# Kernel tuning notes

Measured on AMD Instinct MI355X. Metric: run time of the kernel, lower is better.

Reference implementation:

```python
import jax, jax.numpy as jnp
import numpy as np

HIDDEN = 1024
HEADS = 16
HEAD_DIM = HIDDEN // HEADS  # 64
B, S = 4, 2048


def setup_inputs() -> dict:
    key = jax.random.key(0)
    ks = jax.random.split(key, 8)
    scale = 1.0 / np.sqrt(HIDDEN)
    return {
        "hidden_states": jax.random.normal(ks[0], (B, S, HIDDEN), dtype=jnp.float32),
        "attention_mask": jnp.zeros((B, S), dtype=jnp.float32),  # additive mask: 0 = keep
        "Wq": jax.random.normal(ks[1], (HIDDEN, HIDDEN), dtype=jnp.float32) * scale,
        "bq": jnp.zeros((HIDDEN,), dtype=jnp.float32),
        "Wk": jax.random.normal(ks[2], (HIDDEN, HIDDEN), dtype=jnp.float32) * scale,
        "bk": jnp.zeros((HIDDEN,), dtype=jnp.float32),
        "Wv": jax.random.normal(ks[3], (HIDDEN, HIDDEN), dtype=jnp.float32) * scale,
        "bv": jnp.zeros((HIDDEN,), dtype=jnp.float32),
    }


def reference(hidden_states, attention_mask, Wq, bq, Wk, bk, Wv, bv):
    b, s, _ = hidden_states.shape

    def split_heads(x):  # [b,s,hidden] -> [b,h,s,d]
        return x.reshape(b, s, HEADS, HEAD_DIM).transpose(0, 2, 1, 3)

    q = split_heads(hidden_states @ Wq + bq)
    k = split_heads(hidden_states @ Wk + bk)
    v = split_heads(hidden_states @ Wv + bv)

    # [b,h,s,s] attention scores, scaled, with additive mask broadcast to [b,1,1,s]
    scores = jnp.einsum("bhqd,bhkd->bhqk", q, k) / np.sqrt(HEAD_DIM)
    scores = scores + attention_mask[:, None, None, :]
    probs = jax.nn.softmax(scores, axis=-1)
    # dropout prob = 0 (eval); head_mask=None
    ctx = jnp.einsum("bhqk,bhkd->bhqd", probs, v)  # [b,h,s,d]
    return ctx.transpose(0, 2, 1, 3).reshape(b, s, HIDDEN)
```

## Files before the change

kernel.cpp:

```cpp
#include <hip/hip_runtime.h>
#include <hip/hip_bf16.h>

typedef unsigned short u16t;
typedef unsigned int   u32t;
typedef float  f32x4  __attribute__((ext_vector_type(4)));
typedef __bf16 bf16x8 __attribute__((ext_vector_type(8)));

#define HIDDEN 1024
#define HEADS  16
#define HDIM   64
#define BB     4
#define SS     2048
#define BH     (BB * HEADS)
#define MTOT   (BB * SS)
#define LOG2E  1.4426950408889634f

__device__ inline u16t f2bf(float f) {
  __hip_bfloat16 h = __float2bfloat16(f);
  return *reinterpret_cast<u16t*>(&h);
}

__device__ inline float fast_exp2(float x) {
#if __has_builtin(__builtin_amdgcn_exp2f)
  return __builtin_amdgcn_exp2f(x);
#else
  return exp2f(x);
#endif
}

__device__ inline void gload_lds16(const void* g, void* l) {
  __builtin_amdgcn_global_load_lds(
      (const __attribute__((address_space(1))) void*)g,
      (__attribute__((address_space(3))) void*)l, 16, 0, 0);
}

__global__ __launch_bounds__(256) void k_convert_x(const float* __restrict__ X,
                                                   u16t* __restrict__ Xb, int n4) {
  int i = blockIdx.x * blockDim.x + threadIdx.x;
  int stride = gridDim.x * blockDim.x;
  for (; i < n4; i += stride) {
    float4 v = reinterpret_cast<const float4*>(X)[i];
    ushort4 o;
    o.x = f2bf(v.x); o.y = f2bf(v.y); o.z = f2bf(v.z); o.w = f2bf(v.w);
    reinterpret_cast<ushort4*>(Xb)[i] = o;
  }
}

__global__ __launch_bounds__(256) void k_transpose_w(const float* __restrict__ Wq,
                                                     const float* __restrict__ Wk,
                                                     const float* __restrict__ Wv,
                                                     u16t* __restrict__ Wt) {
  __shared__ float tile[64][65];
  const int mat = blockIdx.z;
  const float* W = (mat == 0) ? Wq : (mat == 1) ? Wk : Wv;
  const int k0 = blockIdx.x * 64, n0 = blockIdx.y * 64;
  const int t = threadIdx.x;
  const int c = t & 63, rbase = t >> 6;
#pragma unroll
  for (int p = 0; p < 16; ++p) {
    int r = p * 4 + rbase;
    tile[r][c] = W[(size_t)(k0 + r) * HIDDEN + n0 + c];
  }
  __syncthreads();
  u16t* Wo = Wt + (size_t)mat * HIDDEN * HIDDEN;
#pragma unroll
  for (int p = 0; p < 16; ++p) {
    int r = p * 4 + rbase;
    Wo[(size_t)(n0 + r) * HIDDEN + k0 + c] = f2bf(tile[c][r]);
  }
}

template <bool SWAP>
__global__ __launch_bounds__(256) void k_qkv_gemm(const u16t* __restrict__ Xb,
                                                  const u16t* __restrict__ Wt,
                                                  const float* __restrict__ bq,
                                                  const float* __restrict__ bk,
                                                  const float* __restrict__ bv,
                                                  u16t* __restrict__ QKV,
                                                  int n0base) {
  __shared__ __align__(16) u16t As[128 * 64];
  __shared__ __align__(16) u16t Bs[128 * 64];
  const int nwg = (int)(gridDim.x * gridDim.y);
  const int bid = (int)(blockIdx.x + gridDim.x * blockIdx.y);
  const int lg  = (bid & 7) * (nwg >> 3) + (bid >> 3);
  const int m0 = (lg & 63) * 128, n0 = n0base + (lg >> 6) * 128;
  const int tid = threadIdx.x;
  const int w = tid >> 6, l = tid & 63;
  const int lq = l & 15, g = l >> 4;
  const int wm = (w >> 1) * 64, wn = (w & 1) * 64;

  f32x4 acc[4][4] = {};

  for (int t = 0; t < 16; ++t) {
    const int k0 = t * 64;
    __syncthreads();
#pragma unroll
    for (int p = 0; p < 4; ++p) {
      int chunk = p * 256 + tid;
      int row = chunk >> 3, c16 = chunk & 7;
      int sc = ((c16 ^ (row & 7)) * 8);
      gload_lds16(Xb + (size_t)(m0 + row) * HIDDEN + k0 + sc,
                  &As[(p * 256 + w * 64) * 8]);
      gload_lds16(Wt + (size_t)(n0 + row) * HIDDEN + k0 + sc,
                  &Bs[(p * 256 + w * 64) * 8]);
    }
    __syncthreads();
#pragma unroll
    for (int kc = 0; kc < 2; ++kc) {
      bf16x8 af[4], bfr[4];
#pragma unroll
      for (int i = 0; i < 4; ++i) {
        int rowA = wm + i * 16 + lq;
        af[i] = *reinterpret_cast<const bf16x8*>(
            &As[rowA * 64 + (((kc * 4 + g) ^ (rowA & 7)) * 8)]);
        int rowB = wn + i * 16 + lq;
        bfr[i] = *reinterpret_cast<const bf16x8*>(
            &Bs[rowB * 64 + (((kc * 4 + g) ^ (rowB & 7)) * 8)]);
      }
#pragma unroll
      for (int i = 0; i < 4; ++i)
#pragma unroll
        for (int j = 0; j < 4; ++j) {
          if constexpr (SWAP)
            acc[i][j] = __builtin_amdgcn_mfma_f32_16x16x32_bf16(bfr[j], af[i],
                                                                acc[i][j], 0, 0, 0);
          else
            acc[i][j] = __builtin_amdgcn_mfma_f32_16x16x32_bf16(af[i], bfr[j],
                                                                acc[i][j], 0, 0, 0);
        }
    }
  }

  if constexpr (SWAP) {
    const int nb_ = n0 >> 10;
    const float* bias = nb_ ? bk : bq;
    const float scl = nb_ ? 1.0f : 0.125f * LOG2E;
#pragma unroll
    for (int j = 0; j < 4; ++j) {
      int nf = (n0 & 1023) + wn + j * 16 + g * 4;
      int h = nf >> 6, d0 = nf & 63;
      float4 b4 = *reinterpret_cast<const float4*>(&bias[nf]);
#pragma unroll
      for (int i = 0; i < 4; ++i) {
        int m = m0 + wm + i * 16 + lq;
        int b = m >> 11, s = m & 2047;
        ushort4 o;
        o.x = f2bf((acc[i][j][0] + b4.x) * scl);
        o.y = f2bf((acc[i][j][1] + b4.y) * scl);
        o.z = f2bf((acc[i][j][2] + b4.z) * scl);
        o.w = f2bf((acc[i][j][3] + b4.w) * scl);
        *reinterpret_cast<ushort4*>(
            &QKV[(((size_t)(nb_ * BH + b * HEADS + h)) * SS + s) * HDIM + d0]) = o;
      }
    }
  } else {
    u16t* Vg = QKV + (size_t)2 * BH * SS * HDIM;
#pragma unroll
    for (int j = 0; j < 4; ++j) {
      int n = (n0 - 2048) + wn + j * 16 + lq;
      int h = n >> 6, d = n & 63;
      float bval = bv[n];
#pragma unroll
      for (int i = 0; i < 4; ++i) {
        int m = m0 + wm + i * 16 + g * 4;
        int b = m >> 11, s = m & 2047;
        int tt = s >> 6, k = s & 63;
        int slot = (k & 32) + ((k >> 2) & 3) * 8 + ((k >> 4) & 1) * 4;
        ushort4 o;
        o.x = f2bf(acc[i][j][0] + bval);
        o.y = f2bf(acc[i][j][1] + bval);
        o.z = f2bf(acc[i][j][2] + bval);
        o.w = f2bf(acc[i][j][3] + bval);
        *reinterpret_cast<ushort4*>(
            &Vg[(((size_t)(b * HEADS + h)) * HDIM + d) * SS + tt * 64 + slot]) = o;
      }
    }
  }
}

__global__ __launch_bounds__(256) void k_attn(const u16t* __restrict__ QKV,
                                              const float* __restrict__ mask,
                                              float* __restrict__ out) {
  __shared__ __align__(16) u16t Ks[2][64 * 64];
  __shared__ __align__(16) u16t Vs[2][64 * 64];
  __shared__ float Ms[SS];
  const int bid = (int)(blockIdx.x + gridDim.x * blockIdx.y);
  const int lg  = (bid & 7) * 128 + (bid >> 3);
  const int qt = lg & 15, bh = lg >> 4;
  const int b = bh >> 4, h = bh & 15;
  const int tid = threadIdx.x, w = tid >> 6, l = tid & 63;
  const int lq = l & 15, g = l >> 4;
  const int q0 = qt * 128 + w * 32;

  const u16t* Qh = QKV + (size_t)bh * SS * HDIM;
  const u16t* Kh = QKV + (size_t)(BH + bh) * SS * HDIM;
  const u16t* Vh = QKV + (size_t)(2 * BH) * SS * HDIM + (size_t)bh * HDIM * SS;

  {
    const float4* m4 = reinterpret_cast<const float4*>(mask + (size_t)b * SS);
    float4* s4 = reinterpret_cast<float4*>(Ms);
    for (int i = tid; i < SS / 4; i += 256) {
      float4 v = m4[i];
      v.x = v.x * LOG2E - 8.0f; v.y = v.y * LOG2E - 8.0f;
      v.z = v.z * LOG2E - 8.0f; v.w = v.w * LOG2E - 8.0f;
      s4[i] = v;
    }
  }

  bf16x8 qf[2][2];
#pragma unroll
  for (int qi = 0; qi < 2; ++qi) {
    qf[qi][0] = *reinterpret_cast<const bf16x8*>(
        &Qh[(size_t)(q0 + qi * 16 + lq) * HDIM + g * 8]);
    qf[qi][1] = *reinterpret_cast<const bf16x8*>(
        &Qh[(size_t)(q0 + qi * 16 + lq) * HDIM + 32 + g * 8]);
  }

  const int cA = tid, cB = 256 + tid;
  const u16t* ksrcA = Kh + (size_t)(cA >> 3) * HDIM + (((cA & 7) ^ ((cA >> 3) & 7)) * 8);
  const u16t* ksrcB = Kh + (size_t)(cB >> 3) * HDIM + (((cB & 7) ^ ((cB >> 3) & 7)) * 8);
  const u16t* vsrcA = Vh + (size_t)(cA >> 3) * SS + (((cA & 7) ^ ((cA >> 3) & 7)) * 8);
  const u16t* vsrcB = Vh + (size_t)(cB >> 3) * SS + (((cB & 7) ^ ((cB >> 3) & 7)) * 8);

  auto STAGE = [&](int t, int bufi) {
    const size_t ko = (size_t)t * 64 * HDIM;
    const int vo = t * 64;
    gload_lds16(ksrcA + ko, &Ks[bufi][(w * 64) * 8]);
    gload_lds16(ksrcB + ko, &Ks[bufi][(256 + w * 64) * 8]);
    gload_lds16(vsrcA + vo, &Vs[bufi][(w * 64) * 8]);
    gload_lds16(vsrcB + vo, &Vs[bufi][(256 + w * 64) * 8]);
  };

  float lsum[2] = {0.f, 0.f};
  f32x4 ctx[2][4] = {};
  u32t pk[2][4][2];

  STAGE(0, 0);
  __syncthreads();

  for (int kv = 0; kv < 32; ++kv) {
    const int cur = kv & 1;
    const int k0 = kv * 64;
    STAGE((kv + 1) & 31, cur ^ 1);
    asm volatile("s_waitcnt vmcnt(4)\n\ts_barrier" ::: "memory");

    const u16t* Kb = &Ks[cur][0];
    const u16t* Vb = &Vs[cur][0];

    bf16x8 kf[4][2];
#pragma unroll
    for (int mt = 0; mt < 4; ++mt) {
      int row = mt * 16 + lq;
      kf[mt][0] = *reinterpret_cast<const bf16x8*>(
          &Kb[row * 64 + ((g ^ (row & 7)) * 8)]);
      kf[mt][1] = *reinterpret_cast<const bf16x8*>(
          &Kb[row * 64 + (((4 + g) ^ (row & 7)) * 8)]);
    }

    float4 mvs[4];
#pragma unroll
    for (int mt = 0; mt < 4; ++mt)
      mvs[mt] = *reinterpret_cast<const float4*>(&Ms[k0 + mt * 16 + g * 4]);

#pragma unroll
    for (int qi = 0; qi < 2; ++qi) {
      f32x4 s[4];
      __builtin_amdgcn_s_setprio(1);
#pragma unroll
      for (int mt = 0; mt < 4; ++mt) {
        f32x4 z = {};
        z = __builtin_amdgcn_mfma_f32_16x16x32_bf16(kf[mt][0], qf[qi][0], z, 0, 0, 0);
        z = __builtin_amdgcn_mfma_f32_16x16x32_bf16(kf[mt][1], qf[qi][1], z, 0, 0, 0);
        s[mt][0] = z[0] + mvs[mt].x; s[mt][1] = z[1] + mvs[mt].y;
        s[mt][2] = z[2] + mvs[mt].z; s[mt][3] = z[3] + mvs[mt].w;
      }
      __builtin_amdgcn_s_setprio(0);
      float ps = 0.f;
#pragma unroll
      for (int mt = 0; mt < 4; ++mt) {
        float p0 = fast_exp2(s[mt][0]), p1 = fast_exp2(s[mt][1]);
        float p2 = fast_exp2(s[mt][2]), p3 = fast_exp2(s[mt][3]);
        ps += (p0 + p1) + (p2 + p3);
        pk[qi][mt][0] = ((u32t)f2bf(p1) << 16) | f2bf(p0);
        pk[qi][mt][1] = ((u32t)f2bf(p3) << 16) | f2bf(p2);
      }
      lsum[qi] += ps;
    }

#pragma unroll
    for (int c = 0; c < 2; ++c) {
      union { u32t u[4]; bf16x8 v; } pb[2];
#pragma unroll
      for (int qi = 0; qi < 2; ++qi) {
        pb[qi].u[0] = pk[qi][2 * c][0];
        pb[qi].u[1] = pk[qi][2 * c][1];
        pb[qi].u[2] = pk[qi][2 * c + 1][0];
        pb[qi].u[3] = pk[qi][2 * c + 1][1];
      }
      __builtin_amdgcn_s_setprio(1);
#pragma unroll
      for (int dt = 0; dt < 4; ++dt) {
        int d = dt * 16 + lq;
        bf16x8 vf = *reinterpret_cast<const bf16x8*>(
            &Vb[d * 64 + (((4 * c + g) ^ (d & 7)) * 8)]);
        ctx[0][dt] = __builtin_amdgcn_mfma_f32_16x16x32_bf16(vf, pb[0].v, ctx[0][dt], 0, 0, 0);
        ctx[1][dt] = __builtin_amdgcn_mfma_f32_16x16x32_bf16(vf, pb[1].v, ctx[1][dt], 0, 0, 0);
      }
      __builtin_amdgcn_s_setprio(0);
    }

    asm volatile("s_barrier" ::: "memory");
  }

#pragma unroll
  for (int qi = 0; qi < 2; ++qi) {
    float ls = lsum[qi];
    ls += __shfl_xor(ls, 16);
    ls += __shfl_xor(ls, 32);
    float rinv = 1.0f / ls;
    int qg = q0 + qi * 16 + lq;
#pragma unroll
    for (int dt = 0; dt < 4; ++dt) {
      float4 o;
      o.x = ctx[qi][dt][0] * rinv; o.y = ctx[qi][dt][1] * rinv;
      o.z = ctx[qi][dt][2] * rinv; o.w = ctx[qi][dt][3] * rinv;
      *reinterpret_cast<float4*>(
          &out[((size_t)(b * SS + qg)) * HIDDEN + h * HDIM + dt * 16 + g * 4]) = o;
    }
  }
}

extern "C" void kernel_launch(void* const* d_in, const int* in_sizes, int n_in,
                              void* d_out, int out_size, void* d_ws, size_t ws_size,
                              hipStream_t stream) {
  const float* X    = (const float*)d_in[0];
  const float* mask = (const float*)d_in[1];
  const float* Wq   = (const float*)d_in[2];
  const float* bq   = (const float*)d_in[3];
  const float* Wk   = (const float*)d_in[4];
  const float* bk   = (const float*)d_in[5];
  const float* Wv   = (const float*)d_in[6];
  const float* bv   = (const float*)d_in[7];
  float* out = (float*)d_out;

  u16t* Xb  = (u16t*)d_ws;
  u16t* Wt  = Xb + (size_t)MTOT * HIDDEN;
  u16t* QKV = Wt + (size_t)3 * HIDDEN * HIDDEN;

  hipLaunchKernelGGL(k_convert_x, dim3(2048), dim3(256), 0, stream,
                     X, Xb, MTOT * HIDDEN / 4);
  hipLaunchKernelGGL(k_transpose_w, dim3(16, 16, 3), dim3(256), 0, stream,
                     Wq, Wk, Wv, Wt);
  hipLaunchKernelGGL((k_qkv_gemm<true>), dim3(64, 16), dim3(256), 0, stream,
                     Xb, Wt, bq, bk, bv, QKV, 0);
  hipLaunchKernelGGL((k_qkv_gemm<false>), dim3(64, 8), dim3(256), 0, stream,
                     Xb, Wt, bq, bk, bv, QKV, 2048);
  hipLaunchKernelGGL(k_attn, dim3(16, 64), dim3(256), 0, stream,
                     QKV, mask, out);
}
```

Measured before the change: 282.0 us.

## Merge QKV GEMM launches and compute softmax row sums with MFMA

New measurement: 274.9 us. 2.5% less time.

```diff
diff --git a/kernel.cpp b/kernel.cpp
--- a/kernel.cpp
+++ b/kernel.cpp
@@ -70,20 +70,19 @@
   }
 }
 
-template <bool SWAP>
 __global__ __launch_bounds__(256) void k_qkv_gemm(const u16t* __restrict__ Xb,
                                                   const u16t* __restrict__ Wt,
                                                   const float* __restrict__ bq,
                                                   const float* __restrict__ bk,
                                                   const float* __restrict__ bv,
-                                                  u16t* __restrict__ QKV,
-                                                  int n0base) {
+                                                  u16t* __restrict__ QKV) {
   __shared__ __align__(16) u16t As[128 * 64];
   __shared__ __align__(16) u16t Bs[128 * 64];
   const int nwg = (int)(gridDim.x * gridDim.y);
   const int bid = (int)(blockIdx.x + gridDim.x * blockIdx.y);
   const int lg  = (bid & 7) * (nwg >> 3) + (bid >> 3);
-  const int m0 = (lg & 63) * 128, n0 = n0base + (lg >> 6) * 128;
+  const int m0 = (lg & 63) * 128, n0 = (lg >> 6) * 128;
+  const bool swp = (n0 < 2048);
   const int tid = threadIdx.x;
   const int w = tid >> 6, l = tid & 63;
   const int lq = l & 15, g = l >> 4;
@@ -117,21 +116,25 @@
         bfr[i] = *reinterpret_cast<const bf16x8*>(
             &Bs[rowB * 64 + (((kc * 4 + g) ^ (rowB & 7)) * 8)]);
       }
-#pragma unroll
-      for (int i = 0; i < 4; ++i)
-#pragma unroll
-        for (int j = 0; j < 4; ++j) {
-          if constexpr (SWAP)
+      if (swp) {
+#pragma unroll
+        for (int i = 0; i < 4; ++i)
+#pragma unroll
+          for (int j = 0; j < 4; ++j)
             acc[i][j] = __builtin_amdgcn_mfma_f32_16x16x32_bf16(bfr[j], af[i],
                                                                 acc[i][j], 0, 0, 0);
-          else
+      } else {
+#pragma unroll
+        for (int i = 0; i < 4; ++i)
+#pragma unroll
+          for (int j = 0; j < 4; ++j)
             acc[i][j] = __builtin_amdgcn_mfma_f32_16x16x32_bf16(af[i], bfr[j],
                                                                 acc[i][j], 0, 0, 0);
-        }
-    }
-  }
-
-  if constexpr (SWAP) {
+      }
+    }
+  }
+
+  if (swp) {
     const int nb_ = n0 >> 10;
     const float* bias = nb_ ? bk : bq;
     const float scl = nb_ ? 1.0f : 0.125f * LOG2E;
@@ -216,6 +219,10 @@
         &Qh[(size_t)(q0 + qi * 16 + lq) * HDIM + 32 + g * 8]);
   }
 
+  union { u32t u[4]; bf16x8 v; } ones;
+#pragma unroll
+  for (int i = 0; i < 4; ++i) ones.u[i] = 0x3F803F80u;
+
   const int cA = tid, cB = 256 + tid;
   const u16t* ksrcA = Kh + (size_t)(cA >> 3) * HDIM + (((cA & 7) ^ ((cA >> 3) & 7)) * 8);
   const u16t* ksrcB = Kh + (size_t)(cB >> 3) * HDIM + (((cB & 7) ^ ((cB >> 3) & 7)) * 8);
@@ -231,8 +238,8 @@
     gload_lds16(vsrcB + vo, &Vs[bufi][(256 + w * 64) * 8]);
   };
 
-  float lsum[2] = {0.f, 0.f};
   f32x4 ctx[2][4] = {};
+  f32x4 psum[2] = {};
   u32t pk[2][4][2];
 
   STAGE(0, 0);
@@ -268,23 +275,19 @@
       __builtin_amdgcn_s_setprio(1);
 #pragma unroll
       for (int mt = 0; mt < 4; ++mt) {
-        f32x4 z = {};
+        f32x4 z = {mvs[mt].x, mvs[mt].y, mvs[mt].z, mvs[mt].w};
         z = __builtin_amdgcn_mfma_f32_16x16x32_bf16(kf[mt][0], qf[qi][0], z, 0, 0, 0);
         z = __builtin_amdgcn_mfma_f32_16x16x32_bf16(kf[mt][1], qf[qi][1], z, 0, 0, 0);
-        s[mt][0] = z[0] + mvs[mt].x; s[mt][1] = z[1] + mvs[mt].y;
-        s[mt][2] = z[2] + mvs[mt].z; s[mt][3] = z[3] + mvs[mt].w;
+        s[mt] = z;
       }
       __builtin_amdgcn_s_setprio(0);
-      float ps = 0.f;
 #pragma unroll
       for (int mt = 0; mt < 4; ++mt) {
         float p0 = fast_exp2(s[mt][0]), p1 = fast_exp2(s[mt][1]);
         float p2 = fast_exp2(s[mt][2]), p3 = fast_exp2(s[mt][3]);
-        ps += (p0 + p1) + (p2 + p3);
         pk[qi][mt][0] = ((u32t)f2bf(p1) << 16) | f2bf(p0);
         pk[qi][mt][1] = ((u32t)f2bf(p3) << 16) | f2bf(p2);
       }
-      lsum[qi] += ps;
     }
 
 #pragma unroll
@@ -306,6 +309,8 @@
         ctx[0][dt] = __builtin_amdgcn_mfma_f32_16x16x32_bf16(vf, pb[0].v, ctx[0][dt], 0, 0, 0);
         ctx[1][dt] = __builtin_amdgcn_mfma_f32_16x16x32_bf16(vf, pb[1].v, ctx[1][dt], 0, 0, 0);
       }
+      psum[0] = __builtin_amdgcn_mfma_f32_16x16x32_bf16(ones.v, pb[0].v, psum[0], 0, 0, 0);
+      psum[1] = __builtin_amdgcn_mfma_f32_16x16x32_bf16(ones.v, pb[1].v, psum[1], 0, 0, 0);
       __builtin_amdgcn_s_setprio(0);
     }
 
@@ -314,10 +319,7 @@
 
 #pragma unroll
   for (int qi = 0; qi < 2; ++qi) {
-    float ls = lsum[qi];
-    ls += __shfl_xor(ls, 16);
-    ls += __shfl_xor(ls, 32);
-    float rinv = 1.0f / ls;
+    float rinv = 1.0f / psum[qi][0];
     int qg = q0 + qi * 16 + lq;
 #pragma unroll
     for (int dt = 0; dt < 4; ++dt) {
@@ -351,10 +353,8 @@
                      X, Xb, MTOT * HIDDEN / 4);
   hipLaunchKernelGGL(k_transpose_w, dim3(16, 16, 3), dim3(256), 0, stream,
                      Wq, Wk, Wv, Wt);
-  hipLaunchKernelGGL((k_qkv_gemm<true>), dim3(64, 16), dim3(256), 0, stream,
-                     Xb, Wt, bq, bk, bv, QKV, 0);
-  hipLaunchKernelGGL((k_qkv_gemm<false>), dim3(64, 8), dim3(256), 0, stream,
-                     Xb, Wt, bq, bk, bv, QKV, 2048);
+  hipLaunchKernelGGL(k_qkv_gemm, dim3(64, 24), dim3(256), 0, stream,
+                     Xb, Wt, bq, bk, bv, QKV);
   hipLaunchKernelGGL(k_attn, dim3(16, 64), dim3(256), 0, stream,
                      QKV, mask, out);
 }
```
